# Kernel optimization log

Measured on AMD Instinct MI355X. Metric: run time of the kernel, lower is better.

The kernel has to match this reference:

```python
import jax, jax.numpy as jnp
import numpy as np

N_NODES = 50000
N_EDGES = 1600000
F = 64
EPS = 1e-05


def setup_inputs() -> dict:
    key = jax.random.key(0)
    k1, k2 = jax.random.split(key)
    e = jax.random.normal(k1, (N_EDGES, F), dtype=jnp.float32)
    dst = jax.random.randint(k2, (N_EDGES,), 0, N_NODES, dtype=jnp.int32)
    gamma = jnp.ones((F,), dtype=jnp.float32)
    beta = jnp.zeros((F,), dtype=jnp.float32)
    return {"e": e, "gamma": gamma, "beta": beta, "dst": dst}


def reference(e, gamma, beta, dst):
    # Per-destination-node statistics over the mailbox [deg, F]:
    #   mean over all deg*F elements; std is torch.std -> unbiased (n-1).
    f = e.shape[1]
    ones = jnp.ones((e.shape[0],), dtype=e.dtype)
    deg = jax.ops.segment_sum(ones, dst, num_segments=N_NODES)          # [N]
    cnt = deg * f                                                        # elements per node
    s = jax.ops.segment_sum(e.sum(axis=-1), dst, num_segments=N_NODES)  # [N]
    ss = jax.ops.segment_sum((e * e).sum(axis=-1), dst, num_segments=N_NODES)
    safe_cnt = jnp.maximum(cnt, 1.0)
    mean = s / safe_cnt
    var = (ss - cnt * mean * mean) / jnp.maximum(cnt - 1.0, 1.0)  # unbiased
    std = jnp.sqrt(jnp.maximum(var, 0.0))
    # Broadcast dst stats back per edge and normalize: (e - mean) / (std + eps)
    norm_e = (e - mean[dst][:, None]) / (std[dst][:, None] + EPS)
    return gamma * norm_e + beta
```

## Files before the change

kernel.cpp:

```cpp
#include <hip/hip_runtime.h>

#define N_NODES_C 50000
#define FDIM 64
#define EPS_C 1e-5f

#define PARTS 16
#define NPP 3125
#define SLICE (3 * NPP)
#define BPERP 48
#define SCAT_BLK 512
#define SCAT_GRID (PARTS * BPERP)

typedef float vfloat4 __attribute__((ext_vector_type(4)));

__device__ __forceinline__ void nt_store_f4(float4* p, float x, float y, float z, float w) {
    vfloat4 v = { x, y, z, w };
    __builtin_nontemporal_store(v, (vfloat4*)p);
}

#define EDGE_ACC(D, SV, QV)                                            \
    { unsigned l_ = (unsigned)((D) - lo);                              \
      if (l_ < NPP) { atomicAdd(&sm[l_], (SV));                        \
                      atomicAdd(&sm[NPP + l_], (QV));                  \
                      atomicAdd(&sm[2 * NPP + l_], 1.0f); } }

__global__ void __launch_bounds__(256)
partial_kernel(const float4* __restrict__ e4, float2* __restrict__ partials,
               int nEdges) {
    const int total = nEdges * 16;
    const int stride = gridDim.x * blockDim.x;
    for (int idx = blockIdx.x * blockDim.x + threadIdx.x; idx < total; idx += stride) {
        float4 v = e4[idx];
        float sum = (v.x + v.y) + (v.z + v.w);
        float sq  = (v.x * v.x + v.y * v.y) + (v.z * v.z + v.w * v.w);
#pragma unroll
        for (int m = 1; m < 16; m <<= 1) {
            sum += __shfl_xor(sum, m);
            sq  += __shfl_xor(sq,  m);
        }
        if ((idx & 15) == 0) {
            unsigned long long bits;
            float2 pq = make_float2(sum, sq);
            __builtin_memcpy(&bits, &pq, 8);
            __builtin_nontemporal_store(bits, (unsigned long long*)(partials + (idx >> 4)));
        }
    }
}

__global__ void __launch_bounds__(SCAT_BLK, 6)
scatter_kernel(const int* __restrict__ dst, const float2* __restrict__ partials,
               float* __restrict__ acc, int nEdges) {
    __shared__ float sm[SLICE];
    const int tid = threadIdx.x;
    for (int i = tid; i < SLICE; i += SCAT_BLK) sm[i] = 0.0f;
    __syncthreads();

    const int p  = blockIdx.x / BPERP;
    const int b  = blockIdx.x % BPERP;
    const int lo = p * NPP;

    const int step = BPERP * SCAT_BLK * 4;
    for (int i0 = (b * SCAT_BLK + tid) * 4; i0 < nEdges; i0 += step) {
        if (i0 + 3 < nEdges) {
            int4   d4  = *(const int4*)(dst + i0);
            float4 p01 = *(const float4*)(partials + i0);
            float4 p23 = *(const float4*)(partials + i0 + 2);
            EDGE_ACC(d4.x, p01.x, p01.y); EDGE_ACC(d4.y, p01.z, p01.w);
            EDGE_ACC(d4.z, p23.x, p23.y); EDGE_ACC(d4.w, p23.z, p23.w);
        } else {
            for (int i = i0; i < nEdges; ++i) {
                float2 pq = partials[i];
                EDGE_ACC(dst[i], pq.x, pq.y);
            }
        }
    }
    __syncthreads();
    float* __restrict__ outp = acc + (size_t)blockIdx.x * SLICE;
    for (int i = tid; i < SLICE; i += SCAT_BLK) {
        __builtin_nontemporal_store(sm[i], outp + i);
    }
}

__global__ void __launch_bounds__(256)
reduce_finalize_kernel(const float* __restrict__ acc, float2* __restrict__ stats,
                       int nNodes) {
    int n = blockIdx.x * blockDim.x + threadIdx.x;
    if (n >= nNodes) return;
    int p = n / NPP, local = n - p * NPP;
    const float* bptr = acc + (size_t)(p * BPERP) * SLICE + local;
    float s = 0.f, q = 0.f, dg = 0.f;
#pragma unroll 8
    for (int bb = 0; bb < BPERP; ++bb, bptr += SLICE) {
        s  += bptr[0];
        q  += bptr[NPP];
        dg += bptr[2 * NPP];
    }
    float cnt  = dg * (float)FDIM;
    float safe = fmaxf(cnt, 1.0f);
    float mean = s / safe;
    float var  = (q - cnt * mean * mean) / fmaxf(cnt - 1.0f, 1.0f);
    float stdv = sqrtf(fmaxf(var, 0.0f));
    stats[n] = make_float2(mean, 1.0f / (stdv + EPS_C));
}

__global__ void __launch_bounds__(256)
norm_kernel(const float4* __restrict__ e4, const int* __restrict__ dst,
            const float2* __restrict__ stats,
            const float4* __restrict__ gamma4, const float4* __restrict__ beta4,
            float4* __restrict__ out4, int nEdges) {
    const int total  = nEdges * 16;
    const int stride = gridDim.x * blockDim.x;
    const int gtid   = blockIdx.x * blockDim.x + threadIdx.x;
    const int sub    = gtid & 15;
    const float4 g = gamma4[sub];
    const float4 b = beta4[sub];
    const int nIter = (total + stride - 1) / stride;
    for (int it = nIter - 1; it >= 0; --it) {
        int idx = it * stride + gtid;
        if (idx >= total) continue;
        float2 mi = stats[dst[idx >> 4]];
        float4 v  = e4[idx];
        nt_store_f4(out4 + idx,
                    g.x * (v.x - mi.x) * mi.y + b.x,
                    g.y * (v.y - mi.x) * mi.y + b.y,
                    g.z * (v.z - mi.x) * mi.y + b.z,
                    g.w * (v.w - mi.x) * mi.y + b.w);
    }
}

extern "C" void kernel_launch(void* const* d_in, const int* in_sizes, int n_in,
                              void* d_out, int out_size, void* d_ws, size_t ws_size,
                              hipStream_t stream) {
    const float* e     = (const float*)d_in[0];
    const float* gamma = (const float*)d_in[1];
    const float* beta  = (const float*)d_in[2];
    const int*   dst   = (const int*)d_in[3];
    const int nEdges = in_sizes[3];
    const int nNodes = N_NODES_C;

    float*  acc      = (float*)d_ws;
    float2* stats    = (float2*)(acc + (size_t)SCAT_GRID * SLICE);
    float2* partials = stats + nNodes;

    partial_kernel<<<2048, 256, 0, stream>>>((const float4*)e, partials, nEdges);
    scatter_kernel<<<SCAT_GRID, SCAT_BLK, 0, stream>>>(dst, partials, acc, nEdges);
    reduce_finalize_kernel<<<(nNodes + 255) / 256, 256, 0, stream>>>(acc, stats, nNodes);
    norm_kernel<<<2048, 256, 0, stream>>>(
        (const float4*)e, dst, stats,
        (const float4*)gamma, (const float4*)beta,
        (float4*)d_out, nEdges);
}
```

Before: 246.9 us.

## Bucketize edges by node partition instead of rescanning all edges per partition

The separate partial-sum pass and the scatter pass, in which every partition's blocks rescanned the full dst and partials arrays, are replaced by two kernels. The first computes per-edge sum and sum-of-squares and appends compact (local index, sum, sq) entries into per-partition, per-shard lists, staged through shared-memory buckets. The second kernel has one block per list that accumulates its entries with shared-memory atomics. This removes the redundant reads of dst and partials across partitions, and the reduce step now sums 8 shards instead of 48. In exchange it adds a memset, global atomics for list offsets, and fixed list capacities (SUBCAP) that would silently drop edges under a skewed dst distribution.

```diff
diff --git a/kernel.cpp b/kernel.cpp
--- a/kernel.cpp
+++ b/kernel.cpp
@@ -7,9 +7,13 @@
 #define PARTS 16
 #define NPP 3125
 #define SLICE (3 * NPP)
-#define BPERP 48
-#define SCAT_BLK 512
-#define SCAT_GRID (PARTS * BPERP)
+#define NSHARD 8
+#define NLIST (PARTS * NSHARD)
+#define SUBCAP 16384
+#define BUK_BLK 512
+#define BUK_GRID 1024
+#define CAP 160
+#define ACC_BLK 512
 
 typedef float vfloat4 __attribute__((ext_vector_type(4)));
 
@@ -18,67 +22,89 @@
     __builtin_nontemporal_store(v, (vfloat4*)p);
 }
 
-#define EDGE_ACC(D, SV, QV)                                            \
-    { unsigned l_ = (unsigned)((D) - lo);                              \
-      if (l_ < NPP) { atomicAdd(&sm[l_], (SV));                        \
-                      atomicAdd(&sm[NPP + l_], (QV));                  \
-                      atomicAdd(&sm[2 * NPP + l_], 1.0f); } }
-
-__global__ void __launch_bounds__(256)
-partial_kernel(const float4* __restrict__ e4, float2* __restrict__ partials,
-               int nEdges) {
-    const int total = nEdges * 16;
-    const int stride = gridDim.x * blockDim.x;
-    for (int idx = blockIdx.x * blockDim.x + threadIdx.x; idx < total; idx += stride) {
-        float4 v = e4[idx];
-        float sum = (v.x + v.y) + (v.z + v.w);
-        float sq  = (v.x * v.x + v.y * v.y) + (v.z * v.z + v.w * v.w);
-#pragma unroll
-        for (int m = 1; m < 16; m <<= 1) {
-            sum += __shfl_xor(sum, m);
-            sq  += __shfl_xor(sq,  m);
-        }
-        if ((idx & 15) == 0) {
-            unsigned long long bits;
-            float2 pq = make_float2(sum, sq);
-            __builtin_memcpy(&bits, &pq, 8);
-            __builtin_nontemporal_store(bits, (unsigned long long*)(partials + (idx >> 4)));
-        }
-    }
-}
-
-__global__ void __launch_bounds__(SCAT_BLK, 6)
-scatter_kernel(const int* __restrict__ dst, const float2* __restrict__ partials,
-               float* __restrict__ acc, int nEdges) {
-    __shared__ float sm[SLICE];
+__global__ void __launch_bounds__(BUK_BLK)
+bucketize_kernel(const float4* __restrict__ e4, const int* __restrict__ dst,
+                 float4* __restrict__ lists, int* __restrict__ gcnt, int nEdges) {
+    __shared__ float4 buk[PARTS][CAP];
+    __shared__ int bcnt[PARTS];
+    __shared__ int flushbase;
     const int tid = threadIdx.x;
-    for (int i = tid; i < SLICE; i += SCAT_BLK) sm[i] = 0.0f;
+    if (tid < PARTS) bcnt[tid] = 0;
     __syncthreads();
 
-    const int p  = blockIdx.x / BPERP;
-    const int b  = blockIdx.x % BPERP;
-    const int lo = p * NPP;
+    const int group = tid >> 4, sub = tid & 15;
+    const int NG  = BUK_GRID * (BUK_BLK / 16);
+    const int gid = blockIdx.x * (BUK_BLK / 16) + group;
+    const int shard = blockIdx.x & (NSHARD - 1);
+    const int R = (nEdges + NG - 1) / NG;
 
-    const int step = BPERP * SCAT_BLK * 4;
-    for (int i0 = (b * SCAT_BLK + tid) * 4; i0 < nEdges; i0 += step) {
-        if (i0 + 3 < nEdges) {
-            int4   d4  = *(const int4*)(dst + i0);
-            float4 p01 = *(const float4*)(partials + i0);
-            float4 p23 = *(const float4*)(partials + i0 + 2);
-            EDGE_ACC(d4.x, p01.x, p01.y); EDGE_ACC(d4.y, p01.z, p01.w);
-            EDGE_ACC(d4.z, p23.x, p23.y); EDGE_ACC(d4.w, p23.z, p23.w);
-        } else {
-            for (int i = i0; i < nEdges; ++i) {
-                float2 pq = partials[i];
-                EDGE_ACC(dst[i], pq.x, pq.y);
+    for (int r = 0; r < R; ++r) {
+        const int edge = gid + r * NG;
+        if (edge < nEdges) {
+            float4 v = e4[(size_t)edge * 16 + sub];
+            float sum = (v.x + v.y) + (v.z + v.w);
+            float sq  = (v.x * v.x + v.y * v.y) + (v.z * v.z + v.w * v.w);
+#pragma unroll
+            for (int m = 1; m < 16; m <<= 1) {
+                sum += __shfl_xor(sum, m);
+                sq  += __shfl_xor(sq,  m);
+            }
+            if (sub == 0) {
+                int d = dst[edge];
+                int p = d / NPP;
+                int local = d - p * NPP;
+                float4 ent;
+                ent.x = __uint_as_float((unsigned)local);
+                ent.y = sum; ent.z = sq; ent.w = 0.0f;
+                int pos = atomicAdd(&bcnt[p], 1);
+                if (pos < CAP) {
+                    buk[p][pos] = ent;
+                } else {
+                    int g = atomicAdd(&gcnt[p * NSHARD + shard], 1);
+                    if (g < SUBCAP)
+                        lists[(size_t)(p * NSHARD + shard) * SUBCAP + g] = ent;
+                }
             }
         }
     }
     __syncthreads();
-    float* __restrict__ outp = acc + (size_t)blockIdx.x * SLICE;
-    for (int i = tid; i < SLICE; i += SCAT_BLK) {
+
+    for (int q = 0; q < PARTS; ++q) {
+        const int c = min(bcnt[q], CAP);
+        if (c > 0) {
+            if (tid == 0) flushbase = atomicAdd(&gcnt[q * NSHARD + shard], c);
+            __syncthreads();
+            const int base = flushbase;
+            float4* dstp = lists + (size_t)(q * NSHARD + shard) * SUBCAP;
+            for (int i = tid; i < c; i += BUK_BLK)
+                if (base + i < SUBCAP) dstp[base + i] = buk[q][i];
+        }
+        __syncthreads();
+    }
+}
+
+__global__ void __launch_bounds__(ACC_BLK)
+accumulate_kernel(const float4* __restrict__ lists, const int* __restrict__ gcnt,
+                  float* __restrict__ acc) {
+    __shared__ float sm[SLICE];
+    const int tid = threadIdx.x;
+    for (int i = tid; i < SLICE; i += ACC_BLK) sm[i] = 0.0f;
+    __syncthreads();
+
+    const int li  = blockIdx.x;
+    const int cnt = min(gcnt[li], SUBCAP);
+    const float4* src = lists + (size_t)li * SUBCAP;
+    for (int i = tid; i < cnt; i += ACC_BLK) {
+        float4 ent = src[i];
+        unsigned l = __float_as_uint(ent.x);
+        atomicAdd(&sm[l], ent.y);
+        atomicAdd(&sm[NPP + l], ent.z);
+        atomicAdd(&sm[2 * NPP + l], 1.0f);
+    }
+    __syncthreads();
+    float* __restrict__ outp = acc + (size_t)li * SLICE;
+    for (int i = tid; i < SLICE; i += ACC_BLK)
         __builtin_nontemporal_store(sm[i], outp + i);
-    }
 }
 
 __global__ void __launch_bounds__(256)
@@ -87,10 +113,10 @@
     int n = blockIdx.x * blockDim.x + threadIdx.x;
     if (n >= nNodes) return;
     int p = n / NPP, local = n - p * NPP;
-    const float* bptr = acc + (size_t)(p * BPERP) * SLICE + local;
+    const float* bptr = acc + (size_t)(p * NSHARD) * SLICE + local;
     float s = 0.f, q = 0.f, dg = 0.f;
-#pragma unroll 8
-    for (int bb = 0; bb < BPERP; ++bb, bptr += SLICE) {
+#pragma unroll
+    for (int ss = 0; ss < NSHARD; ++ss, bptr += SLICE) {
         s  += bptr[0];
         q  += bptr[NPP];
         dg += bptr[2 * NPP];
@@ -138,12 +164,16 @@
     const int nEdges = in_sizes[3];
     const int nNodes = N_NODES_C;
 
-    float*  acc      = (float*)d_ws;
-    float2* stats    = (float2*)(acc + (size_t)SCAT_GRID * SLICE);
-    float2* partials = stats + nNodes;
+    float4* lists = (float4*)d_ws;
+    float*  acc   = (float*)(lists + (size_t)NLIST * SUBCAP);
+    float2* stats = (float2*)(acc + (size_t)NLIST * SLICE);
+    int*    gcnt  = (int*)(stats + nNodes);
 
-    partial_kernel<<<2048, 256, 0, stream>>>((const float4*)e, partials, nEdges);
-    scatter_kernel<<<SCAT_GRID, SCAT_BLK, 0, stream>>>(dst, partials, acc, nEdges);
+    hipMemsetAsync(gcnt, 0, NLIST * sizeof(int), stream);
+
+    bucketize_kernel<<<BUK_GRID, BUK_BLK, 0, stream>>>(
+        (const float4*)e, dst, lists, gcnt, nEdges);
+    accumulate_kernel<<<NLIST, ACC_BLK, 0, stream>>>(lists, gcnt, acc);
     reduce_finalize_kernel<<<(nNodes + 255) / 256, 256, 0, stream>>>(acc, stats, nNodes);
     norm_kernel<<<2048, 256, 0, stream>>>(
         (const float4*)e, dst, stats,
```

New measurement: 352.2 us. 42.7% more time.
